# Performance work log

Hardware: AMD Instinct MI355X
Metric: run time of the kernel (lower is better)

## Reference

```python
import jax, jax.numpy as jnp
import numpy as np
from jax import lax

H = 32  # hidden size

def _lstm_layer(x, w_ih, w_hh):
    # x: [B, T, D]; w_ih: [4H, D]; w_hh: [4H, H]; no biases.
    B, T, _ = x.shape
    # Precompute input contributions for all timesteps (one big GEMM).
    xg = jnp.einsum('btd,gd->btg', x, w_ih)  # [B, T, 4H]
    h0 = jnp.zeros((B, H), x.dtype)
    c0 = jnp.zeros((B, H), x.dtype)

    def step(carry, xg_t):
        h, c = carry
        gates = xg_t + h @ w_hh.T  # [B, 4H]
        i, f, g, o = jnp.split(gates, 4, axis=-1)  # PyTorch gate order i,f,g,o
        i = jax.nn.sigmoid(i)
        f = jax.nn.sigmoid(f)
        g = jnp.tanh(g)
        o = jax.nn.sigmoid(o)
        c = f * c + i * g
        h = o * jnp.tanh(c)
        return (h, c), h

    _, hs = lax.scan(step, (h0, c0), jnp.swapaxes(xg, 0, 1))  # hs: [T, B, H]
    return jnp.swapaxes(hs, 0, 1)  # [B, T, H]

def setup_inputs() -> dict:
    key = jax.random.key(0)
    ks = jax.random.split(key, 7)
    B, T, D = 4096, 512, 28
    s = lambda *sh: 0.1  # small init scale for stability over long scans
    return {
        'x':     jax.random.normal(ks[0], (B, T, D), jnp.float32),
        'w_ih0': jax.random.normal(ks[1], (4 * H, D), jnp.float32) * 0.1,
        'w_hh0': jax.random.normal(ks[2], (4 * H, H), jnp.float32) * 0.1,
        'w_ih1': jax.random.normal(ks[3], (4 * H, H), jnp.float32) * 0.1,
        'w_hh1': jax.random.normal(ks[4], (4 * H, H), jnp.float32) * 0.1,
        'w_out': jax.random.normal(ks[5], (10, H), jnp.float32) * 0.1,
        'b_out': jax.random.normal(ks[6], (10,), jnp.float32) * 0.1,
    }

def reference(x, w_ih0, w_hh0, w_ih1, w_hh1, w_out, b_out):
    h1 = _lstm_layer(x, w_ih0, w_hh0)   # layer 0 output [B, T, H]
    # Dropout(0.8) between layers is identity in eval mode.
    h2 = _lstm_layer(h1, w_ih1, w_hh1)  # layer 1 output [B, T, H]
    last = h2[:, -1, :]                  # [B, H]
    return last @ w_out.T + b_out        # [B, 10]
```

## Files before the change

### kernel.cpp

```cpp
#include <hip/hip_runtime.h>
#include <hip/hip_bf16.h>


#define T_LEN 512
#define D_IN  28

typedef __attribute__((ext_vector_type(8))) short short8;
typedef __attribute__((ext_vector_type(4))) float f32x4;
typedef __attribute__((ext_vector_type(4))) unsigned int u32x4;

#define K_SIG 1.4426950408889634f
#define K_TANH 2.8853900817779268f

__device__ __forceinline__ void split_bf16(float x, short& hi, short& lo) {
  unsigned u = __float_as_uint(x);
  hi = (short)(u >> 16);
  float hf_ = __uint_as_float(u & 0xFFFF0000u);
  float lf = x - hf_;
  lo = (short)(__float_as_uint(lf) >> 16);
}

__device__ __forceinline__ unsigned pk_hi16(float f1, float f0) {
  return __builtin_amdgcn_perm(__float_as_uint(f1), __float_as_uint(f0),
                               0x07060302u);
}
__device__ __forceinline__ float trunc_bf(float f) {
  return __uint_as_float(__float_as_uint(f) & 0xFFFF0000u);
}

__device__ __forceinline__ void lds_barrier() {
  asm volatile("s_waitcnt lgkmcnt(0)\n\ts_barrier" ::: "memory");
}

__device__ __forceinline__ void load_wtile(const float* __restrict__ W, int ldk,
                                           int kval, int n, int lane,
                                           short8& hi, short8& lo) {
  int row = n * 16 + (lane & 15);
  int kb = (lane >> 4) * 8;
  const float* p = W + row * ldk + kb;
#pragma unroll
  for (int i = 0; i < 8; ++i) {
    float v = (kb + i < kval) ? p[i] : 0.0f;
    short h, l;
    split_bf16(v, h, l);
    hi[i] = h; lo[i] = l;
  }
}

#define MFMA(a, b, c) __builtin_amdgcn_mfma_f32_16x16x32_bf16(a, b, c, 0, 0, 0)

__device__ __forceinline__ void gate_mfma(f32x4* acc, short8 ah, short8 al,
                                          const short8* Bh, const short8* Bl,
                                          short8 ch, short8 cl,
                                          const short8* Dh, const short8* Dl) {
#pragma unroll
  for (int tt = 0; tt < 4; ++tt) {
    f32x4 z = {0.f, 0.f, 0.f, 0.f};
    acc[tt] = MFMA(ah, Bh[tt], z);
  }
#pragma unroll
  for (int tt = 0; tt < 4; ++tt) acc[tt] = MFMA(al, Bh[tt], acc[tt]);
#pragma unroll
  for (int tt = 0; tt < 4; ++tt) acc[tt] = MFMA(ah, Bl[tt], acc[tt]);
#pragma unroll
  for (int tt = 0; tt < 4; ++tt) acc[tt] = MFMA(ch, Dh[tt], acc[tt]);
#pragma unroll
  for (int tt = 0; tt < 4; ++tt) acc[tt] = MFMA(cl, Dh[tt], acc[tt]);
#pragma unroll
  for (int tt = 0; tt < 4; ++tt) acc[tt] = MFMA(ch, Dl[tt], acc[tt]);
}

__device__ __forceinline__ void cell_update(const f32x4* acc, float* c, float* h) {
  float ei[4], ef[4], eg[4], eo[4];
#pragma unroll
  for (int r = 0; r < 4; ++r) {
    ei[r] = __builtin_amdgcn_exp2f(acc[0][r] * -K_SIG);
    ef[r] = __builtin_amdgcn_exp2f(acc[1][r] * -K_SIG);
    eg[r] = __builtin_amdgcn_exp2f(acc[2][r] * K_TANH);
    eo[r] = __builtin_amdgcn_exp2f(acc[3][r] * -K_SIG);
  }
  float cn[4];
#pragma unroll
  for (int r = 0; r < 4; ++r) {
    float pig = (1.0f + ei[r]) * (1.0f + eg[r]);
    float num = c[r] * pig + (eg[r] - 1.0f) * (1.0f + ef[r]);
    cn[r] = num * __builtin_amdgcn_rcpf(pig * (1.0f + ef[r]));
  }
  float ec[4];
#pragma unroll
  for (int r = 0; r < 4; ++r) ec[r] = __builtin_amdgcn_exp2f(cn[r] * K_TANH);
#pragma unroll
  for (int r = 0; r < 4; ++r) {
    float R2 = __builtin_amdgcn_rcpf((1.0f + eo[r]) * (1.0f + ec[r]));
    c[r] = cn[r];
    h[r] = (ec[r] - 1.0f) * R2;
  }
}

template <int P>
__device__ __forceinline__ void l1_half(
    float4& A0, float4& A1, const float* __restrict__ ld,
    const short8* Wxh, const short8* Wxl, const short8* Whh_, const short8* Whl,
    short (*h1)[2][16][40], float* c, float* h,
    int lrow, int lgrp, int kb, int uu) {
  constexpr int Q = P ^ 1;
  short8 ph = *(const short8*)&h1[Q][0][lrow][kb];
  short8 pl = *(const short8*)&h1[Q][1][lrow][kb];

  u32x4 xhu, xlu;
  xhu[0] = pk_hi16(A0.y, A0.x);
  xhu[1] = pk_hi16(A0.w, A0.z);
  xhu[2] = pk_hi16(A1.y, A1.x);
  xhu[3] = pk_hi16(A1.w, A1.z);
  float l0 = A0.x - trunc_bf(A0.x), l1 = A0.y - trunc_bf(A0.y);
  float l2 = A0.z - trunc_bf(A0.z), l3 = A0.w - trunc_bf(A0.w);
  float l4 = A1.x - trunc_bf(A1.x), l5 = A1.y - trunc_bf(A1.y);
  float l6 = A1.z - trunc_bf(A1.z), l7 = A1.w - trunc_bf(A1.w);
  xlu[0] = pk_hi16(l1, l0);
  xlu[1] = pk_hi16(l3, l2);
  xlu[2] = pk_hi16(l5, l4);
  xlu[3] = pk_hi16(l7, l6);
  short8 xh = __builtin_bit_cast(short8, xhu);
  short8 xl = __builtin_bit_cast(short8, xlu);

  A0 = *(const float4*)(ld);
  if (lgrp < 3) A1 = *(const float4*)(ld + 4);

  f32x4 acc[4];
  gate_mfma(acc, xh, xl, Wxh, Wxl, ph, pl, Whh_, Whl);
  cell_update(acc, c, h);
#pragma unroll
  for (int r = 0; r < 4; ++r) {
    short hh_, ll_;
    split_bf16(h[r], hh_, ll_);
    int row = lgrp * 4 + r;
    h1[P][0][row][uu] = hh_;
    h1[P][1][row][uu] = ll_;
  }
}

template <int P>
__device__ __forceinline__ void l2_half(
    const short8* Wxh, const short8* Wxl, const short8* Whh_, const short8* Whl,
    short (*h1)[2][16][40], short (*h2)[2][16][40], float* c, float* h,
    int lrow, int lgrp, int kb, int uu, bool writeout) {
  constexpr int Q = P ^ 1;
  short8 ah = *(const short8*)&h1[Q][0][lrow][kb];
  short8 al = *(const short8*)&h1[Q][1][lrow][kb];
  short8 ph = *(const short8*)&h2[Q][0][lrow][kb];
  short8 pl = *(const short8*)&h2[Q][1][lrow][kb];
  f32x4 acc[4];
  gate_mfma(acc, ah, al, Wxh, Wxl, ph, pl, Whh_, Whl);
  cell_update(acc, c, h);
  if (writeout) {
#pragma unroll
    for (int r = 0; r < 4; ++r) {
      short hh_, ll_;
      split_bf16(h[r], hh_, ll_);
      int row = lgrp * 4 + r;
      h2[P][0][row][uu] = hh_;
      h2[P][1][row][uu] = ll_;
    }
  }
}

__global__ __launch_bounds__(256) void lstm2_pipe(
    const float* __restrict__ x, const float* __restrict__ wih0,
    const float* __restrict__ whh0, const float* __restrict__ wih1,
    const float* __restrict__ whh1, const float* __restrict__ wout,
    const float* __restrict__ bout, float* __restrict__ out) {
  __shared__ short h1buf[2][2][16][40];
  __shared__ short h2buf[2][2][16][40];
  __shared__ float hf[16][33];

  const int tid = threadIdx.x;
  const int lane = tid & 63;
  const int wid = tid >> 6;
  const int layer = wid >> 1;
  const int w01 = wid & 1;
  const int b0 = blockIdx.x * 16;

  for (int i = tid; i < 2 * 2 * 16 * 40; i += 256) {
    ((short*)h1buf)[i] = 0;
    ((short*)h2buf)[i] = 0;
  }

  const int lrow = lane & 15;
  const int lgrp = lane >> 4;
  const int kb = lgrp * 8;
  const int uu = lrow + 16 * w01;

  const float* Wih = layer ? wih1 : wih0;
  const float* Whh = layer ? whh1 : whh0;
  const int ldk = layer ? 32 : 28;

  short8 Wxh[4], Wxl[4], Whh_[4], Whl[4];
#pragma unroll
  for (int tt = 0; tt < 4; ++tt) {
    int n = tt * 2 + w01;
    load_wtile(Wih, ldk, ldk, n, lane, Wxh[tt], Wxl[tt]);
    load_wtile(Whh, 32, 32, n, lane, Whh_[tt], Whl[tt]);
  }

  float c[4] = {0, 0, 0, 0}, h[4] = {0, 0, 0, 0};

  const float* xrow = x + ((size_t)(b0 + lrow)) * T_LEN * D_IN + kb;

  float4 X0A0 = make_float4(0, 0, 0, 0), X0A1 = make_float4(0, 0, 0, 0);
  float4 X1A0 = make_float4(0, 0, 0, 0), X1A1 = make_float4(0, 0, 0, 0);
  if (layer == 0) {
    X0A0 = *(const float4*)(xrow);
    if (lgrp < 3) X0A1 = *(const float4*)(xrow + 4);
    X1A0 = *(const float4*)(xrow + D_IN);
    if (lgrp < 3) X1A1 = *(const float4*)(xrow + D_IN + 4);
  }

  __syncthreads();

  for (int s = 0; s < T_LEN; s += 2) {
    {
      int t2 = s + 2 < T_LEN ? s + 2 : T_LEN - 1;
      const float* ld = xrow + (size_t)t2 * D_IN;
      if (layer == 0) {
        l1_half<0>(X0A0, X0A1, ld, Wxh, Wxl, Whh_, Whl, h1buf, c, h,
                   lrow, lgrp, kb, uu);
      } else if (s > 0) {
        l2_half<0>(Wxh, Wxl, Whh_, Whl, h1buf, h2buf, c, h,
                   lrow, lgrp, kb, uu, true);
      }
      lds_barrier();
    }
    {
      int t3 = s + 3 < T_LEN ? s + 3 : T_LEN - 1;
      const float* ld = xrow + (size_t)t3 * D_IN;
      if (layer == 0) {
        l1_half<1>(X1A0, X1A1, ld, Wxh, Wxl, Whh_, Whl, h1buf, c, h,
                   lrow, lgrp, kb, uu);
      } else {
        l2_half<1>(Wxh, Wxl, Whh_, Whl, h1buf, h2buf, c, h,
                   lrow, lgrp, kb, uu, true);
      }
      lds_barrier();
    }
  }

  if (layer == 1) {
    l2_half<0>(Wxh, Wxl, Whh_, Whl, h1buf, h2buf, c, h,
               lrow, lgrp, kb, uu, false);
#pragma unroll
    for (int r = 0; r < 4; ++r) hf[lgrp * 4 + r][uu] = h[r];
  }
  __syncthreads();

  for (int j = tid; j < 160; j += 256) {
    int row = j / 10, col = j % 10;
    float s = bout[col];
#pragma unroll
    for (int u = 0; u < 32; ++u) s += hf[row][u] * wout[col * 32 + u];
    out[(size_t)(b0 + row) * 10 + col] = s;
  }
}

extern "C" void kernel_launch(void* const* d_in, const int* in_sizes, int n_in,
                              void* d_out, int out_size, void* d_ws, size_t ws_size,
                              hipStream_t stream) {
  const float* x = (const float*)d_in[0];
  const float* wih0 = (const float*)d_in[1];
  const float* whh0 = (const float*)d_in[2];
  const float* wih1 = (const float*)d_in[3];
  const float* whh1 = (const float*)d_in[4];
  const float* wout = (const float*)d_in[5];
  const float* bout = (const float*)d_in[6];
  float* out = (float*)d_out;
  lstm2_pipe<<<256, 256, 0, stream>>>(x, wih0, whh0, wih1, whh1, wout, bout, out);
}
```

Before: 323.3 us.

## Precompute next-step input-side MFMAs off the recurrent critical path and batch reciprocals

```diff
diff --git a/kernel.cpp b/kernel.cpp
--- a/kernel.cpp
+++ b/kernel.cpp
@@ -49,64 +49,8 @@
 
 #define MFMA(a, b, c) __builtin_amdgcn_mfma_f32_16x16x32_bf16(a, b, c, 0, 0, 0)
 
-__device__ __forceinline__ void gate_mfma(f32x4* acc, short8 ah, short8 al,
-                                          const short8* Bh, const short8* Bl,
-                                          short8 ch, short8 cl,
-                                          const short8* Dh, const short8* Dl) {
-#pragma unroll
-  for (int tt = 0; tt < 4; ++tt) {
-    f32x4 z = {0.f, 0.f, 0.f, 0.f};
-    acc[tt] = MFMA(ah, Bh[tt], z);
-  }
-#pragma unroll
-  for (int tt = 0; tt < 4; ++tt) acc[tt] = MFMA(al, Bh[tt], acc[tt]);
-#pragma unroll
-  for (int tt = 0; tt < 4; ++tt) acc[tt] = MFMA(ah, Bl[tt], acc[tt]);
-#pragma unroll
-  for (int tt = 0; tt < 4; ++tt) acc[tt] = MFMA(ch, Dh[tt], acc[tt]);
-#pragma unroll
-  for (int tt = 0; tt < 4; ++tt) acc[tt] = MFMA(cl, Dh[tt], acc[tt]);
-#pragma unroll
-  for (int tt = 0; tt < 4; ++tt) acc[tt] = MFMA(ch, Dl[tt], acc[tt]);
-}
-
-__device__ __forceinline__ void cell_update(const f32x4* acc, float* c, float* h) {
-  float ei[4], ef[4], eg[4], eo[4];
-#pragma unroll
-  for (int r = 0; r < 4; ++r) {
-    ei[r] = __builtin_amdgcn_exp2f(acc[0][r] * -K_SIG);
-    ef[r] = __builtin_amdgcn_exp2f(acc[1][r] * -K_SIG);
-    eg[r] = __builtin_amdgcn_exp2f(acc[2][r] * K_TANH);
-    eo[r] = __builtin_amdgcn_exp2f(acc[3][r] * -K_SIG);
-  }
-  float cn[4];
-#pragma unroll
-  for (int r = 0; r < 4; ++r) {
-    float pig = (1.0f + ei[r]) * (1.0f + eg[r]);
-    float num = c[r] * pig + (eg[r] - 1.0f) * (1.0f + ef[r]);
-    cn[r] = num * __builtin_amdgcn_rcpf(pig * (1.0f + ef[r]));
-  }
-  float ec[4];
-#pragma unroll
-  for (int r = 0; r < 4; ++r) ec[r] = __builtin_amdgcn_exp2f(cn[r] * K_TANH);
-#pragma unroll
-  for (int r = 0; r < 4; ++r) {
-    float R2 = __builtin_amdgcn_rcpf((1.0f + eo[r]) * (1.0f + ec[r]));
-    c[r] = cn[r];
-    h[r] = (ec[r] - 1.0f) * R2;
-  }
-}
-
-template <int P>
-__device__ __forceinline__ void l1_half(
-    float4& A0, float4& A1, const float* __restrict__ ld,
-    const short8* Wxh, const short8* Wxl, const short8* Whh_, const short8* Whl,
-    short (*h1)[2][16][40], float* c, float* h,
-    int lrow, int lgrp, int kb, int uu) {
-  constexpr int Q = P ^ 1;
-  short8 ph = *(const short8*)&h1[Q][0][lrow][kb];
-  short8 pl = *(const short8*)&h1[Q][1][lrow][kb];
-
+__device__ __forceinline__ void pack_xfrag(const float4& A0, const float4& A1,
+                                           short8& xh, short8& xl) {
   u32x4 xhu, xlu;
   xhu[0] = pk_hi16(A0.y, A0.x);
   xhu[1] = pk_hi16(A0.w, A0.z);
@@ -120,14 +64,82 @@
   xlu[1] = pk_hi16(l3, l2);
   xlu[2] = pk_hi16(l5, l4);
   xlu[3] = pk_hi16(l7, l6);
-  short8 xh = __builtin_bit_cast(short8, xhu);
-  short8 xl = __builtin_bit_cast(short8, xlu);
-
-  A0 = *(const float4*)(ld);
-  if (lgrp < 3) A1 = *(const float4*)(ld + 4);
+  xh = __builtin_bit_cast(short8, xhu);
+  xl = __builtin_bit_cast(short8, xlu);
+}
+
+__device__ __forceinline__ void xside_mfma(f32x4* xacc, short8 xh, short8 xl,
+                                           const short8* Bh, const short8* Bl) {
+#pragma unroll
+  for (int tt = 0; tt < 4; ++tt) {
+    f32x4 z = {0.f, 0.f, 0.f, 0.f};
+    xacc[tt] = MFMA(xh, Bh[tt], z);
+  }
+#pragma unroll
+  for (int tt = 0; tt < 4; ++tt) xacc[tt] = MFMA(xl, Bh[tt], xacc[tt]);
+#pragma unroll
+  for (int tt = 0; tt < 4; ++tt) xacc[tt] = MFMA(xh, Bl[tt], xacc[tt]);
+}
+
+__device__ __forceinline__ void cell_update(const f32x4* acc, float* c, float* h) {
+  float ei[4], ef[4], eg[4], eo[4];
+#pragma unroll
+  for (int r = 0; r < 4; ++r) {
+    ei[r] = __builtin_amdgcn_exp2f(acc[0][r] * -K_SIG);
+    ef[r] = __builtin_amdgcn_exp2f(acc[1][r] * -K_SIG);
+    eg[r] = __builtin_amdgcn_exp2f(acc[2][r] * K_TANH);
+    eo[r] = __builtin_amdgcn_exp2f(acc[3][r] * -K_SIG);
+  }
+  float num[4], D[4];
+#pragma unroll
+  for (int r = 0; r < 4; ++r) {
+    float pig = (1.0f + ei[r]) * (1.0f + eg[r]);
+    num[r] = c[r] * pig + (eg[r] - 1.0f) * (1.0f + ef[r]);
+    D[r] = pig * (1.0f + ef[r]);
+  }
+  float R01 = __builtin_amdgcn_rcpf(D[0] * D[1]);
+  float R23 = __builtin_amdgcn_rcpf(D[2] * D[3]);
+  float cn[4];
+  cn[0] = num[0] * D[1] * R01;
+  cn[1] = num[1] * D[0] * R01;
+  cn[2] = num[2] * D[3] * R23;
+  cn[3] = num[3] * D[2] * R23;
+  float ec[4], E[4];
+#pragma unroll
+  for (int r = 0; r < 4; ++r) ec[r] = __builtin_amdgcn_exp2f(cn[r] * K_TANH);
+#pragma unroll
+  for (int r = 0; r < 4; ++r) E[r] = (1.0f + eo[r]) * (1.0f + ec[r]);
+  float S01 = __builtin_amdgcn_rcpf(E[0] * E[1]);
+  float S23 = __builtin_amdgcn_rcpf(E[2] * E[3]);
+  c[0] = cn[0]; h[0] = (ec[0] - 1.0f) * E[1] * S01;
+  c[1] = cn[1]; h[1] = (ec[1] - 1.0f) * E[0] * S01;
+  c[2] = cn[2]; h[2] = (ec[2] - 1.0f) * E[3] * S23;
+  c[3] = cn[3]; h[3] = (ec[3] - 1.0f) * E[2] * S23;
+}
+
+template <int P>
+__device__ __forceinline__ void l1_half(
+    float4& NA0, float4& NA1, const float* __restrict__ ld, f32x4* xacc,
+    const short8* Wxh, const short8* Wxl, const short8* Whh_, const short8* Whl,
+    short (*h1)[2][16][40], float* c, float* h,
+    int lrow, int lgrp, int kb, int uu) {
+  constexpr int Q = P ^ 1;
+  short8 ph = *(const short8*)&h1[Q][0][lrow][kb];
+  short8 pl = *(const short8*)&h1[Q][1][lrow][kb];
+
+  short8 xh, xl;
+  pack_xfrag(NA0, NA1, xh, xl);
+  NA0 = *(const float4*)(ld);
+  if (lgrp < 3) NA1 = *(const float4*)(ld + 4);
 
   f32x4 acc[4];
-  gate_mfma(acc, xh, xl, Wxh, Wxl, ph, pl, Whh_, Whl);
+#pragma unroll
+  for (int tt = 0; tt < 4; ++tt) acc[tt] = MFMA(ph, Whh_[tt], xacc[tt]);
+#pragma unroll
+  for (int tt = 0; tt < 4; ++tt) acc[tt] = MFMA(pl, Whh_[tt], acc[tt]);
+#pragma unroll
+  for (int tt = 0; tt < 4; ++tt) acc[tt] = MFMA(ph, Whl[tt], acc[tt]);
+
   cell_update(acc, c, h);
 #pragma unroll
   for (int r = 0; r < 4; ++r) {
@@ -137,6 +149,8 @@
     h1[P][0][row][uu] = hh_;
     h1[P][1][row][uu] = ll_;
   }
+
+  xside_mfma(xacc, xh, xl, Wxh, Wxl);
 }
 
 template <int P>
@@ -150,7 +164,22 @@
   short8 ph = *(const short8*)&h2[Q][0][lrow][kb];
   short8 pl = *(const short8*)&h2[Q][1][lrow][kb];
   f32x4 acc[4];
-  gate_mfma(acc, ah, al, Wxh, Wxl, ph, pl, Whh_, Whl);
+#pragma unroll
+  for (int tt = 0; tt < 4; ++tt) {
+    f32x4 z = {0.f, 0.f, 0.f, 0.f};
+    acc[tt] = MFMA(ah, Wxh[tt], z);
+  }
+#pragma unroll
+  for (int tt = 0; tt < 4; ++tt) acc[tt] = MFMA(al, Wxh[tt], acc[tt]);
+#pragma unroll
+  for (int tt = 0; tt < 4; ++tt) acc[tt] = MFMA(ah, Wxl[tt], acc[tt]);
+#pragma unroll
+  for (int tt = 0; tt < 4; ++tt) acc[tt] = MFMA(ph, Whh_[tt], acc[tt]);
+#pragma unroll
+  for (int tt = 0; tt < 4; ++tt) acc[tt] = MFMA(pl, Whh_[tt], acc[tt]);
+#pragma unroll
+  for (int tt = 0; tt < 4; ++tt) acc[tt] = MFMA(ph, Whl[tt], acc[tt]);
+
   cell_update(acc, c, h);
   if (writeout) {
 #pragma unroll
@@ -206,23 +235,30 @@
 
   const float* xrow = x + ((size_t)(b0 + lrow)) * T_LEN * D_IN + kb;
 
-  float4 X0A0 = make_float4(0, 0, 0, 0), X0A1 = make_float4(0, 0, 0, 0);
-  float4 X1A0 = make_float4(0, 0, 0, 0), X1A1 = make_float4(0, 0, 0, 0);
+  float4 XOA0 = make_float4(0, 0, 0, 0), XOA1 = make_float4(0, 0, 0, 0);
+  float4 XEA0 = make_float4(0, 0, 0, 0), XEA1 = make_float4(0, 0, 0, 0);
+  f32x4 xacc[4];
   if (layer == 0) {
-    X0A0 = *(const float4*)(xrow);
-    if (lgrp < 3) X0A1 = *(const float4*)(xrow + 4);
-    X1A0 = *(const float4*)(xrow + D_IN);
-    if (lgrp < 3) X1A1 = *(const float4*)(xrow + D_IN + 4);
+    float4 Z0 = *(const float4*)(xrow);
+    float4 Z1 = make_float4(0, 0, 0, 0);
+    if (lgrp < 3) Z1 = *(const float4*)(xrow + 4);
+    XOA0 = *(const float4*)(xrow + D_IN);
+    if (lgrp < 3) XOA1 = *(const float4*)(xrow + D_IN + 4);
+    XEA0 = *(const float4*)(xrow + 2 * D_IN);
+    if (lgrp < 3) XEA1 = *(const float4*)(xrow + 2 * D_IN + 4);
+    short8 xh0, xl0;
+    pack_xfrag(Z0, Z1, xh0, xl0);
+    xside_mfma(xacc, xh0, xl0, Wxh, Wxl);
   }
 
   __syncthreads();
 
   for (int s = 0; s < T_LEN; s += 2) {
     {
-      int t2 = s + 2 < T_LEN ? s + 2 : T_LEN - 1;
-      const float* ld = xrow + (size_t)t2 * D_IN;
+      int t3 = s + 3 < T_LEN ? s + 3 : T_LEN - 1;
+      const float* ld = xrow + (size_t)t3 * D_IN;
       if (layer == 0) {
-        l1_half<0>(X0A0, X0A1, ld, Wxh, Wxl, Whh_, Whl, h1buf, c, h,
+        l1_half<0>(XOA0, XOA1, ld, xacc, Wxh, Wxl, Whh_, Whl, h1buf, c, h,
                    lrow, lgrp, kb, uu);
       } else if (s > 0) {
         l2_half<0>(Wxh, Wxl, Whh_, Whl, h1buf, h2buf, c, h,
@@ -231,10 +267,10 @@
       lds_barrier();
     }
     {
-      int t3 = s + 3 < T_LEN ? s + 3 : T_LEN - 1;
-      const float* ld = xrow + (size_t)t3 * D_IN;
+      int t4 = s + 4 < T_LEN ? s + 4 : T_LEN - 1;
+      const float* ld = xrow + (size_t)t4 * D_IN;
       if (layer == 0) {
-        l1_half<1>(X1A0, X1A1, ld, Wxh, Wxl, Whh_, Whl, h1buf, c, h,
+        l1_half<1>(XEA0, XEA1, ld, xacc, Wxh, Wxl, Whh_, Whl, h1buf, c, h,
                    lrow, lgrp, kb, uu);
       } else {
         l2_half<1>(Wxh, Wxl, Whh_, Whl, h1buf, h2buf, c, h,
```

After: 352.6 us. 1.09x slower.

## Halve batch rows per block and double grid to fill all CUs

Applied to the files above, without the earlier changes.

```diff
diff --git a/kernel.cpp b/kernel.cpp
--- a/kernel.cpp
+++ b/kernel.cpp
@@ -49,64 +49,8 @@
 
 #define MFMA(a, b, c) __builtin_amdgcn_mfma_f32_16x16x32_bf16(a, b, c, 0, 0, 0)
 
-__device__ __forceinline__ void gate_mfma(f32x4* acc, short8 ah, short8 al,
-                                          const short8* Bh, const short8* Bl,
-                                          short8 ch, short8 cl,
-                                          const short8* Dh, const short8* Dl) {
-#pragma unroll
-  for (int tt = 0; tt < 4; ++tt) {
-    f32x4 z = {0.f, 0.f, 0.f, 0.f};
-    acc[tt] = MFMA(ah, Bh[tt], z);
-  }
-#pragma unroll
-  for (int tt = 0; tt < 4; ++tt) acc[tt] = MFMA(al, Bh[tt], acc[tt]);
-#pragma unroll
-  for (int tt = 0; tt < 4; ++tt) acc[tt] = MFMA(ah, Bl[tt], acc[tt]);
-#pragma unroll
-  for (int tt = 0; tt < 4; ++tt) acc[tt] = MFMA(ch, Dh[tt], acc[tt]);
-#pragma unroll
-  for (int tt = 0; tt < 4; ++tt) acc[tt] = MFMA(cl, Dh[tt], acc[tt]);
-#pragma unroll
-  for (int tt = 0; tt < 4; ++tt) acc[tt] = MFMA(ch, Dl[tt], acc[tt]);
-}
-
-__device__ __forceinline__ void cell_update(const f32x4* acc, float* c, float* h) {
-  float ei[4], ef[4], eg[4], eo[4];
-#pragma unroll
-  for (int r = 0; r < 4; ++r) {
-    ei[r] = __builtin_amdgcn_exp2f(acc[0][r] * -K_SIG);
-    ef[r] = __builtin_amdgcn_exp2f(acc[1][r] * -K_SIG);
-    eg[r] = __builtin_amdgcn_exp2f(acc[2][r] * K_TANH);
-    eo[r] = __builtin_amdgcn_exp2f(acc[3][r] * -K_SIG);
-  }
-  float cn[4];
-#pragma unroll
-  for (int r = 0; r < 4; ++r) {
-    float pig = (1.0f + ei[r]) * (1.0f + eg[r]);
-    float num = c[r] * pig + (eg[r] - 1.0f) * (1.0f + ef[r]);
-    cn[r] = num * __builtin_amdgcn_rcpf(pig * (1.0f + ef[r]));
-  }
-  float ec[4];
-#pragma unroll
-  for (int r = 0; r < 4; ++r) ec[r] = __builtin_amdgcn_exp2f(cn[r] * K_TANH);
-#pragma unroll
-  for (int r = 0; r < 4; ++r) {
-    float R2 = __builtin_amdgcn_rcpf((1.0f + eo[r]) * (1.0f + ec[r]));
-    c[r] = cn[r];
-    h[r] = (ec[r] - 1.0f) * R2;
-  }
-}
-
-template <int P>
-__device__ __forceinline__ void l1_half(
-    float4& A0, float4& A1, const float* __restrict__ ld,
-    const short8* Wxh, const short8* Wxl, const short8* Whh_, const short8* Whl,
-    short (*h1)[2][16][40], float* c, float* h,
-    int lrow, int lgrp, int kb, int uu) {
-  constexpr int Q = P ^ 1;
-  short8 ph = *(const short8*)&h1[Q][0][lrow][kb];
-  short8 pl = *(const short8*)&h1[Q][1][lrow][kb];
-
+__device__ __forceinline__ void pack_xfrag(const float4& A0, const float4& A1,
+                                           short8& xh, short8& xl) {
   u32x4 xhu, xlu;
   xhu[0] = pk_hi16(A0.y, A0.x);
   xhu[1] = pk_hi16(A0.w, A0.z);
@@ -120,73 +64,142 @@
   xlu[1] = pk_hi16(l3, l2);
   xlu[2] = pk_hi16(l5, l4);
   xlu[3] = pk_hi16(l7, l6);
-  short8 xh = __builtin_bit_cast(short8, xhu);
-  short8 xl = __builtin_bit_cast(short8, xlu);
-
+  xh = __builtin_bit_cast(short8, xhu);
+  xl = __builtin_bit_cast(short8, xlu);
+}
+
+__device__ __forceinline__ void gate_mfma(f32x4* acc, short8 ah, short8 al,
+                                          const short8* Bh, const short8* Bl,
+                                          short8 ch, short8 cl,
+                                          const short8* Dh, const short8* Dl) {
+#pragma unroll
+  for (int tt = 0; tt < 4; ++tt) {
+    f32x4 z = {0.f, 0.f, 0.f, 0.f};
+    acc[tt] = MFMA(ah, Bh[tt], z);
+  }
+#pragma unroll
+  for (int tt = 0; tt < 4; ++tt) acc[tt] = MFMA(al, Bh[tt], acc[tt]);
+#pragma unroll
+  for (int tt = 0; tt < 4; ++tt) acc[tt] = MFMA(ah, Bl[tt], acc[tt]);
+#pragma unroll
+  for (int tt = 0; tt < 4; ++tt) acc[tt] = MFMA(ch, Dh[tt], acc[tt]);
+#pragma unroll
+  for (int tt = 0; tt < 4; ++tt) acc[tt] = MFMA(cl, Dh[tt], acc[tt]);
+#pragma unroll
+  for (int tt = 0; tt < 4; ++tt) acc[tt] = MFMA(ch, Dl[tt], acc[tt]);
+}
+
+__device__ __forceinline__ void cell2(const f32x4* acc, bool hi2,
+                                      float* c, float* h) {
+  float g0[2], g1[2], g2[2], g3[2];
+#pragma unroll
+  for (int j = 0; j < 2; ++j) {
+    g0[j] = hi2 ? acc[0][2 + j] : acc[0][j];
+    g1[j] = hi2 ? acc[1][2 + j] : acc[1][j];
+    g2[j] = hi2 ? acc[2][2 + j] : acc[2][j];
+    g3[j] = hi2 ? acc[3][2 + j] : acc[3][j];
+  }
+  float ei[2], ef[2], eg[2], eo[2];
+#pragma unroll
+  for (int j = 0; j < 2; ++j) {
+    ei[j] = __builtin_amdgcn_exp2f(g0[j] * -K_SIG);
+    ef[j] = __builtin_amdgcn_exp2f(g1[j] * -K_SIG);
+    eg[j] = __builtin_amdgcn_exp2f(g2[j] * K_TANH);
+    eo[j] = __builtin_amdgcn_exp2f(g3[j] * -K_SIG);
+  }
+  float num[2], D[2];
+#pragma unroll
+  for (int j = 0; j < 2; ++j) {
+    float pig = (1.0f + ei[j]) * (1.0f + eg[j]);
+    num[j] = c[j] * pig + (eg[j] - 1.0f) * (1.0f + ef[j]);
+    D[j] = pig * (1.0f + ef[j]);
+  }
+  float R = __builtin_amdgcn_rcpf(D[0] * D[1]);
+  float cn0 = num[0] * D[1] * R;
+  float cn1 = num[1] * D[0] * R;
+  float ec0 = __builtin_amdgcn_exp2f(cn0 * K_TANH);
+  float ec1 = __builtin_amdgcn_exp2f(cn1 * K_TANH);
+  float E0 = (1.0f + eo[0]) * (1.0f + ec0);
+  float E1 = (1.0f + eo[1]) * (1.0f + ec1);
+  float S = __builtin_amdgcn_rcpf(E0 * E1);
+  c[0] = cn0; h[0] = (ec0 - 1.0f) * E1 * S;
+  c[1] = cn1; h[1] = (ec1 - 1.0f) * E0 * S;
+}
+
+__device__ __forceinline__ void store_h2cells(short (*hb)[8][40], const float* h,
+                                              int lgrp, bool hi2, int uu) {
+#pragma unroll
+  for (int j = 0; j < 2; ++j) {
+    short hh_, ll_;
+    split_bf16(h[j], hh_, ll_);
+    int bj = (4 * lgrp + (hi2 ? 2 : 0) + j) & 7;
+    hb[0][bj][uu] = hh_;
+    hb[1][bj][uu] = ll_;
+  }
+}
+
+template <int P>
+__device__ __forceinline__ void l1_half(
+    float4& A0, float4& A1, const float* __restrict__ ld,
+    const short8* Wxh, const short8* Wxl, const short8* Whh_, const short8* Whl,
+    short (*h1)[2][8][40], float* c, float* h,
+    int brow, int lgrp, bool hi2, int kb, int uu) {
+  constexpr int Q = P ^ 1;
+  short8 ph = *(const short8*)&h1[Q][0][brow][kb];
+  short8 pl = *(const short8*)&h1[Q][1][brow][kb];
+
+  short8 xh, xl;
+  pack_xfrag(A0, A1, xh, xl);
   A0 = *(const float4*)(ld);
   if (lgrp < 3) A1 = *(const float4*)(ld + 4);
 
   f32x4 acc[4];
   gate_mfma(acc, xh, xl, Wxh, Wxl, ph, pl, Whh_, Whl);
-  cell_update(acc, c, h);
-#pragma unroll
-  for (int r = 0; r < 4; ++r) {
-    short hh_, ll_;
-    split_bf16(h[r], hh_, ll_);
-    int row = lgrp * 4 + r;
-    h1[P][0][row][uu] = hh_;
-    h1[P][1][row][uu] = ll_;
-  }
+  cell2(acc, hi2, c, h);
+  store_h2cells(h1[P], h, lgrp, hi2, uu);
 }
 
 template <int P>
 __device__ __forceinline__ void l2_half(
     const short8* Wxh, const short8* Wxl, const short8* Whh_, const short8* Whl,
-    short (*h1)[2][16][40], short (*h2)[2][16][40], float* c, float* h,
-    int lrow, int lgrp, int kb, int uu, bool writeout) {
+    short (*h1)[2][8][40], short (*h2)[2][8][40], float* c, float* h,
+    int brow, int lgrp, bool hi2, int kb, int uu, bool writeout) {
   constexpr int Q = P ^ 1;
-  short8 ah = *(const short8*)&h1[Q][0][lrow][kb];
-  short8 al = *(const short8*)&h1[Q][1][lrow][kb];
-  short8 ph = *(const short8*)&h2[Q][0][lrow][kb];
-  short8 pl = *(const short8*)&h2[Q][1][lrow][kb];
+  short8 ah = *(const short8*)&h1[Q][0][brow][kb];
+  short8 al = *(const short8*)&h1[Q][1][brow][kb];
+  short8 ph = *(const short8*)&h2[Q][0][brow][kb];
+  short8 pl = *(const short8*)&h2[Q][1][brow][kb];
   f32x4 acc[4];
   gate_mfma(acc, ah, al, Wxh, Wxl, ph, pl, Whh_, Whl);
-  cell_update(acc, c, h);
-  if (writeout) {
-#pragma unroll
-    for (int r = 0; r < 4; ++r) {
-      short hh_, ll_;
-      split_bf16(h[r], hh_, ll_);
-      int row = lgrp * 4 + r;
-      h2[P][0][row][uu] = hh_;
-      h2[P][1][row][uu] = ll_;
-    }
-  }
-}
-
-__global__ __launch_bounds__(256) void lstm2_pipe(
+  cell2(acc, hi2, c, h);
+  if (writeout) store_h2cells(h2[P], h, lgrp, hi2, uu);
+}
+
+__global__ __launch_bounds__(256, 2) void lstm2_pipe(
     const float* __restrict__ x, const float* __restrict__ wih0,
     const float* __restrict__ whh0, const float* __restrict__ wih1,
     const float* __restrict__ whh1, const float* __restrict__ wout,
     const float* __restrict__ bout, float* __restrict__ out) {
-  __shared__ short h1buf[2][2][16][40];
-  __shared__ short h2buf[2][2][16][40];
-  __shared__ float hf[16][33];
+  __shared__ short h1buf[2][2][8][40];
+  __shared__ short h2buf[2][2][8][40];
+  __shared__ float hf[8][33];
 
   const int tid = threadIdx.x;
   const int lane = tid & 63;
   const int wid = tid >> 6;
   const int layer = wid >> 1;
   const int w01 = wid & 1;
-  const int b0 = blockIdx.x * 16;
-
-  for (int i = tid; i < 2 * 2 * 16 * 40; i += 256) {
+  const int b0 = blockIdx.x * 8;
+
+  for (int i = tid; i < 2 * 2 * 8 * 40; i += 256) {
     ((short*)h1buf)[i] = 0;
     ((short*)h2buf)[i] = 0;
   }
 
   const int lrow = lane & 15;
+  const int brow = lrow & 7;
   const int lgrp = lane >> 4;
+  const bool hi2 = (lgrp >= 2);
   const int kb = lgrp * 8;
   const int uu = lrow + 16 * w01;
 
@@ -202,9 +215,9 @@
     load_wtile(Whh, 32, 32, n, lane, Whh_[tt], Whl[tt]);
   }
 
-  float c[4] = {0, 0, 0, 0}, h[4] = {0, 0, 0, 0};
-
-  const float* xrow = x + ((size_t)(b0 + lrow)) * T_LEN * D_IN + kb;
+  float c[2] = {0, 0}, h[2] = {0, 0};
+
+  const float* xrow = x + ((size_t)(b0 + brow)) * T_LEN * D_IN + kb;
 
   float4 X0A0 = make_float4(0, 0, 0, 0), X0A1 = make_float4(0, 0, 0, 0);
   float4 X1A0 = make_float4(0, 0, 0, 0), X1A1 = make_float4(0, 0, 0, 0);
@@ -223,10 +236,10 @@
       const float* ld = xrow + (size_t)t2 * D_IN;
       if (layer == 0) {
         l1_half<0>(X0A0, X0A1, ld, Wxh, Wxl, Whh_, Whl, h1buf, c, h,
-                   lrow, lgrp, kb, uu);
+                   brow, lgrp, hi2, kb, uu);
       } else if (s > 0) {
         l2_half<0>(Wxh, Wxl, Whh_, Whl, h1buf, h2buf, c, h,
-                   lrow, lgrp, kb, uu, true);
+                   brow, lgrp, hi2, kb, uu, true);
       }
       lds_barrier();
     }
@@ -235,10 +248,10 @@
       const float* ld = xrow + (size_t)t3 * D_IN;
       if (layer == 0) {
         l1_half<1>(X1A0, X1A1, ld, Wxh, Wxl, Whh_, Whl, h1buf, c, h,
-                   lrow, lgrp, kb, uu);
+                   brow, lgrp, hi2, kb, uu);
       } else {
         l2_half<1>(Wxh, Wxl, Whh_, Whl, h1buf, h2buf, c, h,
-                   lrow, lgrp, kb, uu, true);
+                   brow, lgrp, hi2, kb, uu, true);
       }
       lds_barrier();
     }
@@ -246,13 +259,16 @@
 
   if (layer == 1) {
     l2_half<0>(Wxh, Wxl, Whh_, Whl, h1buf, h2buf, c, h,
-               lrow, lgrp, kb, uu, false);
-#pragma unroll
-    for (int r = 0; r < 4; ++r) hf[lgrp * 4 + r][uu] = h[r];
+               brow, lgrp, hi2, kb, uu, false);
+#pragma unroll
+    for (int j = 0; j < 2; ++j) {
+      int bj = (4 * lgrp + (hi2 ? 2 : 0) + j) & 7;
+      hf[bj][uu] = h[j];
+    }
   }
   __syncthreads();
 
-  for (int j = tid; j < 160; j += 256) {
+  for (int j = tid; j < 80; j += 256) {
     int row = j / 10, col = j % 10;
     float s = bout[col];
 #pragma unroll
@@ -272,5 +288,5 @@
   const float* wout = (const float*)d_in[5];
   const float* bout = (const float*)d_in[6];
   float* out = (float*)d_out;
-  lstm2_pipe<<<256, 256, 0, stream>>>(x, wih0, whh0, wih1, whh1, wout, bout, out);
-}
+  lstm2_pipe<<<512, 256, 0, stream>>>(x, wih0, whh0, wih1, whh1, wout, bout, out);
+}
```

New measurement: 404.8 us. 1.25x slower.
